# Kernel tuning notes

Measured on AMD Instinct MI355X. Metric: run time of the kernel, lower is better.

## Reference

```python
import jax, jax.numpy as jnp
import numpy as np

B, C, H, W = 8, 256, 64, 64
CI = 128  # inter_channels = in_channels // reduction

def _conv1x1(x, w, b):
    # x: [b, c, h, w], w: [o, c], b: [o]
    return jnp.einsum('bchw,oc->bohw', x, w) + b[None, :, None, None]

def setup_inputs() -> dict:
    key = jax.random.key(0)
    ks = jax.random.split(key, 5)
    s_in = 1.0 / np.sqrt(C)
    s_ci = 1.0 / np.sqrt(CI)
    return {
        'x': jax.random.normal(ks[0], (B, C, H, W), jnp.float32),
        'w_g': jax.random.normal(ks[1], (CI, C), jnp.float32) * s_in,
        'b_g': jnp.zeros((CI,), jnp.float32),
        'w_theta': jax.random.normal(ks[2], (CI, C), jnp.float32) * s_in,
        'b_theta': jnp.zeros((CI,), jnp.float32),
        'w_phi': jax.random.normal(ks[3], (CI, C), jnp.float32) * s_in,
        'b_phi': jnp.zeros((CI,), jnp.float32),
        'w_out': jax.random.normal(ks[4], (C, CI), jnp.float32) * s_ci,
        'b_out': jnp.zeros((C,), jnp.float32),
    }

def reference(x, w_g, b_g, w_theta, b_theta, w_phi, b_phi, w_out, b_out):
    n, c, h, w = x.shape
    N = h * w
    g_x = _conv1x1(x, w_g, b_g).reshape(n, CI, N).transpose(0, 2, 1)        # [b, N, ci]
    theta_x = _conv1x1(x, w_theta, b_theta).reshape(n, CI, N).transpose(0, 2, 1)  # [b, N, ci]
    phi_x = _conv1x1(x, w_phi, b_phi).reshape(n, CI, N)                     # [b, ci, N]
    pw = jnp.einsum('bnc,bcm->bnm', theta_x, phi_x)                         # [b, N, N]
    # Faithful to source: divides by ci**(-0.5) == multiplies by sqrt(ci)
    pw = pw / (jnp.asarray(CI, x.dtype) ** -0.5)
    pw = jax.nn.softmax(pw, axis=-1)
    y = jnp.einsum('bnm,bmc->bnc', pw, g_x)                                 # [b, N, ci]
    y = y.transpose(0, 2, 1).reshape(n, CI, h, w)
    return x + _conv1x1(y, w_out, b_out)
```

## Files before the change

kernel.cpp:

```cpp
#include <hip/hip_runtime.h>
#include <hip/hip_bf16.h>
#include <stdint.h>
#include <stddef.h>


typedef __bf16 bf16;
typedef __attribute__((ext_vector_type(8))) __bf16 bf16x8;
typedef __attribute__((ext_vector_type(4))) __bf16 bf16x4;
typedef __attribute__((ext_vector_type(4))) float  f32x4;
typedef __attribute__((ext_vector_type(4))) int    i32x4;

#define MFMA16(a, b, c) __builtin_amdgcn_mfma_f32_16x16x32_bf16((a), (b), (c), 0, 0, 0)

constexpr int NB  = 8;
constexpr int NC  = 256;
constexpr int NN  = 4096;
constexpr int NCI = 128;
constexpr size_t NEL = (size_t)NB * NN * NCI;
constexpr int PBATCH = NN * NCI;

#define QSCALE (11.313708498984761f * 1.4426950408889634f)


__global__ __launch_bounds__(256) void k_proj3(
    const float* __restrict__ x,
    const float* __restrict__ wt, const float* __restrict__ bt,
    const float* __restrict__ wp, const float* __restrict__ bp,
    const float* __restrict__ wg, const float* __restrict__ bg,
    bf16* __restrict__ qh, bf16* __restrict__ ql,
    bf16* __restrict__ kh, bf16* __restrict__ kl,
    bf16* __restrict__ vv)
{
    const int nt  = blockIdx.x;
    const int b   = blockIdx.y;
    const int tid = threadIdx.x;
    const int wv  = tid >> 6;
    const int ln  = tid & 63;
    const int lg  = ln >> 4;
    const int lq  = ln & 15;

    __shared__ char lds[49152];
    char* Ah = lds;
    char* Al = lds + 8192;
    char* Wh = lds + 16384;
    char* Wl = lds + 32768;

    f32x4 acc[3][8];
#pragma unroll
    for (int pj = 0; pj < 3; ++pj)
#pragma unroll
        for (int j = 0; j < 8; ++j) acc[pj][j] = f32x4{0.f, 0.f, 0.f, 0.f};

    const int n0 = nt * 64;

    for (int c0 = 0; c0 < NC; c0 += 64) {
        __syncthreads();
#pragma unroll
        for (int p = 0; p < 4; ++p) {
            int cc = p * 16 + (tid >> 4);
            int nn = (tid & 15) * 4;
            f32x4 xv = *(const f32x4*)(x + ((size_t)b * NC + (c0 + cc)) * NN + n0 + nn);
#pragma unroll
            for (int e = 0; e < 4; ++e) {
                float f = xv[e];
                bf16 hh = (bf16)f;
                int row = nn + e;
                int off = (row * 128 + cc * 2) ^ ((row & 7) << 4);
                *(bf16*)(Ah + off) = hh;
                *(bf16*)(Al + off) = (bf16)(f - (float)hh);
            }
        }

#pragma unroll
        for (int pj = 0; pj < 3; ++pj) {
            const float* W = (pj == 0) ? wt : (pj == 1) ? wp : wg;
            const bool split = (pj != 2);
            if (pj != 0) __syncthreads();
#pragma unroll
            for (int p = 0; p < 8; ++p) {
                int i  = p * 16 + (tid >> 4);
                int c4 = (tid & 15) * 4;
                f32x4 w4 = *(const f32x4*)(W + (size_t)i * NC + c0 + c4);
                bf16x4 hv, lv;
#pragma unroll
                for (int e = 0; e < 4; ++e) {
                    bf16 hh = (bf16)w4[e];
                    hv[e] = hh;
                    lv[e] = (bf16)(w4[e] - (float)hh);
                }
                int off = (i * 128 + c4 * 2) ^ ((i & 7) << 4);
                *(bf16x4*)(Wh + off) = hv;
                if (split) *(bf16x4*)(Wl + off) = lv;
            }
            __syncthreads();
#pragma unroll
            for (int kk = 0; kk < 2; ++kk) {
                int row  = wv * 16 + lq;
                int koff = kk * 64 + lg * 16;
                int aoff = (row * 128 + koff) ^ ((row & 7) << 4);
                bf16x8 ah = *(const bf16x8*)(Ah + aoff);
                bf16x8 al = *(const bf16x8*)(Al + aoff);
#pragma unroll
                for (int j = 0; j < 8; ++j) {
                    int ir   = j * 16 + lq;
                    int woff = (ir * 128 + koff) ^ ((ir & 7) << 4);
                    bf16x8 bh = *(const bf16x8*)(Wh + woff);
                    acc[pj][j] = MFMA16(ah, bh, acc[pj][j]);
                    if (split) {
                        bf16x8 bl = *(const bf16x8*)(Wl + woff);
                        acc[pj][j] = MFMA16(ah, bl, acc[pj][j]);
                        acc[pj][j] = MFMA16(al, bh, acc[pj][j]);
                    }
                }
            }
        }
    }

#pragma unroll
    for (int j = 0; j < 8; ++j) {
        int i = j * 16 + lq;
        float bvt = bt[i];
        float bvp = bp[i];
#pragma unroll
        for (int r = 0; r < 4; ++r) {
            int q = n0 + wv * 16 + lg * 4 + r;
            size_t off = ((size_t)b * NN + q) * NCI + i;
            float vt2 = (acc[0][j][r] + bvt) * QSCALE;
            bf16 th = (bf16)vt2;
            qh[off] = th; ql[off] = (bf16)(vt2 - (float)th);
            float vp2 = acc[1][j][r] + bvp;
            bf16 phh = (bf16)vp2;
            kh[off] = phh; kl[off] = (bf16)(vp2 - (float)phh);
        }
    }

    __syncthreads();
    char* T = lds;
#pragma unroll
    for (int j = 0; j < 8; ++j) {
        int i = j * 16 + lq;
        float bv2 = bg[i];
#pragma unroll
        for (int r = 0; r < 4; ++r) {
            int nl = wv * 16 + lg * 4 + r;
            int off = (i * 128 + nl * 2) ^ ((i & 7) << 4);
            *(bf16*)(T + off) = (bf16)(acc[2][j][r] + bv2);
        }
    }
    __syncthreads();
#pragma unroll
    for (int p = 0; p < 4; ++p) {
        int i  = p * 32 + (tid >> 3);
        int sl = tid & 7;
        i32x4 tv = *(const i32x4*)(T + ((i * 128 + sl * 16) ^ ((i & 7) << 4)));
        size_t off = (size_t)b * PBATCH
                   + (size_t)((((nt * 8 + (i >> 4)) * 2 + (sl >> 2)) * 64
                               + (sl & 3) * 16 + (i & 15)) * 8);
        *(i32x4*)(vv + off) = tv;
    }
}

__global__ __launch_bounds__(128, 2) void k_attn_sp(
    const bf16* __restrict__ qh, const bf16* __restrict__ ql,
    const bf16* __restrict__ kh, const bf16* __restrict__ kl,
    const bf16* __restrict__ vf,
    bf16* __restrict__ p0, bf16* __restrict__ p1, float* __restrict__ ml)
{
    const int bid = blockIdx.x;
    const int b   = bid & 7;
    const int rs  = bid >> 3;
    const int qt  = rs & 63;
    const int h   = rs >> 6;
    const int tid = threadIdx.x;
    const int wv  = tid >> 6;
    const int ln  = tid & 63;
    const int lg  = ln >> 4;
    const int lq  = ln & 15;
    const int n0  = qt * 64;
    const int mb0 = h * 2048;
    bf16* ph = h ? p1 : p0;

    __shared__ __attribute__((aligned(16))) char lds[36864];
    char* P = lds + 32768 + wv * 2048;

    const int smm = tid >> 4;
    const int ssl = tid & 15;

    bf16x8 qhf[2][4], qlf[2][4];
#pragma unroll
    for (int q2 = 0; q2 < 2; ++q2) {
        int qrow = n0 + wv * 32 + q2 * 16 + lq;
        const bf16* bh = qh + ((size_t)b * NN + qrow) * NCI;
        const bf16* bl = ql + ((size_t)b * NN + qrow) * NCI;
#pragma unroll
        for (int kk = 0; kk < 4; ++kk) {
            qhf[q2][kk] = *(const bf16x8*)(bh + kk * 32 + lg * 8);
            qlf[q2][kk] = *(const bf16x8*)(bl + kk * 32 + lg * 8);
        }
    }

    f32x4 o[2][8];
#pragma unroll
    for (int q2 = 0; q2 < 2; ++q2)
#pragma unroll
        for (int j = 0; j < 8; ++j) o[q2][j] = f32x4{0.f, 0.f, 0.f, 0.f};
    float mrun[2] = {-1e30f, -1e30f};
    float lrun[2] = {0.f, 0.f};

    const bf16* vb = vf + (size_t)b * PBATCH + (size_t)ln * 8;

    {
#pragma unroll
        for (int p = 0; p < 4; ++p) {
            int mm = p * 8 + smm;
            size_t g = ((size_t)b * NN + mb0 + mm) * NCI + ssl * 8;
            i32x4 hv = *(const i32x4*)(kh + g);
            i32x4 lv = *(const i32x4*)(kl + g);
            int off = (mm * 256 + ssl * 16) ^ ((mm & 7) << 4);
            *(i32x4*)(lds + off) = hv;
            *(i32x4*)(lds + 8192 + off) = lv;
        }
    }
    __syncthreads();

    for (int t = 0; t < 64; ++t) {
        const int cur = t & 1;
        char* KHc = lds + cur * 16384;
        char* KLc = KHc + 8192;
        char* KHn = lds + (cur ^ 1) * 16384;
        char* KLn = KHn + 8192;
        const bool pre = (t < 63);

        i32x4 rkh[4], rkl[4];
        if (pre) {
#pragma unroll
            for (int p = 0; p < 4; ++p) {
                size_t g = ((size_t)b * NN + mb0 + (t + 1) * 32 + p * 8 + smm) * NCI + ssl * 8;
                rkh[p] = *(const i32x4*)(kh + g);
                rkl[p] = *(const i32x4*)(kl + g);
            }
        }
        __builtin_amdgcn_sched_barrier(0);

        f32x4 s[2][2];
        __builtin_amdgcn_s_setprio(1);
#pragma unroll
        for (int jm = 0; jm < 2; ++jm) {
            s[jm][0] = f32x4{0.f, 0.f, 0.f, 0.f};
            s[jm][1] = f32x4{0.f, 0.f, 0.f, 0.f};
            const int mrow = jm * 16 + lq;
            const int sw = (mrow & 7) << 4;
#pragma unroll
            for (int kk = 0; kk < 4; ++kk) {
                int aoff = (mrow * 256 + kk * 64 + lg * 16) ^ sw;
                bf16x8 ah = *(const bf16x8*)(KHc + aoff);
                bf16x8 al = *(const bf16x8*)(KLc + aoff);
                s[jm][0] = MFMA16(ah, qhf[0][kk], s[jm][0]);
                s[jm][1] = MFMA16(ah, qhf[1][kk], s[jm][1]);
                s[jm][0] = MFMA16(al, qhf[0][kk], s[jm][0]);
                s[jm][1] = MFMA16(al, qhf[1][kk], s[jm][1]);
                s[jm][0] = MFMA16(ah, qlf[0][kk], s[jm][0]);
                s[jm][1] = MFMA16(ah, qlf[1][kk], s[jm][1]);
            }
        }
        __builtin_amdgcn_s_setprio(0);

        bf16x8 bv[8];
        {
            const bf16* vp = vb + (size_t)(h * 32 + (t >> 1)) * 8192;
#pragma unroll
            for (int j = 0; j < 8; ++j)
                bv[j] = *(const bf16x8*)(vp + (j * 2 + (t & 1)) * 512);
        }
        __builtin_amdgcn_sched_barrier(0);

        if (pre) {
#pragma unroll
            for (int p = 0; p < 4; ++p) {
                int mm = p * 8 + smm;
                int off = (mm * 256 + ssl * 16) ^ ((mm & 7) << 4);
                *(i32x4*)(KHn + off) = rkh[p];
                *(i32x4*)(KLn + off) = rkl[p];
            }
        }

        float tm[2];
        tm[0] = s[0][0][0];
        tm[1] = s[0][1][0];
#pragma unroll
        for (int jm = 0; jm < 2; ++jm)
#pragma unroll
            for (int r = 0; r < 4; ++r) {
                tm[0] = fmaxf(tm[0], s[jm][0][r]);
                tm[1] = fmaxf(tm[1], s[jm][1][r]);
            }
#pragma unroll
        for (int q2 = 0; q2 < 2; ++q2) {
            tm[q2] = fmaxf(tm[q2], __shfl_xor(tm[q2], 16));
            tm[q2] = fmaxf(tm[q2], __shfl_xor(tm[q2], 32));
        }

        bool grow = (tm[0] > mrun[0] + 8.f) || (tm[1] > mrun[1] + 8.f);
        if (__any(grow)) {
            float alpha[2];
#pragma unroll
            for (int q2 = 0; q2 < 2; ++q2) {
                float mnew = fmaxf(mrun[q2], tm[q2]);
                alpha[q2] = exp2f(mrun[q2] - mnew);
                mrun[q2] = mnew;
                lrun[q2] *= alpha[q2];
            }
            float av0[4], av1[4];
#pragma unroll
            for (int r = 0; r < 4; ++r) {
                av0[r] = __shfl(alpha[0], lg * 4 + r);
                av1[r] = __shfl(alpha[1], lg * 4 + r);
            }
#pragma unroll
            for (int j = 0; j < 8; ++j)
#pragma unroll
                for (int r = 0; r < 4; ++r) {
                    o[0][j][r] *= av0[r];
                    o[1][j][r] *= av1[r];
                }
        }

        float psum[2] = {0.f, 0.f};
#pragma unroll
        for (int jm = 0; jm < 2; ++jm)
#pragma unroll
            for (int q2 = 0; q2 < 2; ++q2) {
                bf16x4 pk;
#pragma unroll
                for (int r = 0; r < 4; ++r) {
                    float e2 = exp2f(s[jm][q2][r] - mrun[q2]);
                    psum[q2] += e2;
                    pk[r] = (bf16)e2;
                }
                int row = q2 * 16 + lq;
                int off = (row * 64 + (jm * 16 + lg * 4) * 2) ^ ((row & 7) << 4);
                *(bf16x4*)(P + off) = pk;
            }
#pragma unroll
        for (int q2 = 0; q2 < 2; ++q2) {
            psum[q2] += __shfl_xor(psum[q2], 16);
            psum[q2] += __shfl_xor(psum[q2], 32);
            lrun[q2] += psum[q2];
        }

        bf16x8 pa[2];
#pragma unroll
        for (int q2 = 0; q2 < 2; ++q2) {
            int row = q2 * 16 + lq;
            pa[q2] = *(const bf16x8*)(P + ((row * 64 + lg * 16) ^ ((row & 7) << 4)));
        }
        __builtin_amdgcn_s_setprio(1);
#pragma unroll
        for (int j = 0; j < 8; ++j) {
            o[0][j] = MFMA16(pa[0], bv[j], o[0][j]);
            o[1][j] = MFMA16(pa[1], bv[j], o[1][j]);
        }
        __builtin_amdgcn_s_setprio(0);

        __syncthreads();
    }

    float rl0[4], rl1[4];
#pragma unroll
    for (int r = 0; r < 4; ++r) {
        rl0[r] = 1.f / __shfl(lrun[0], lg * 4 + r);
        rl1[r] = 1.f / __shfl(lrun[1], lg * 4 + r);
    }
#pragma unroll
    for (int j = 0; j < 8; ++j) {
        int d = j * 16 + lq;
#pragma unroll
        for (int r = 0; r < 4; ++r) {
            int q0 = n0 + wv * 32 + lg * 4 + r;
            ph[((size_t)b * NN + q0) * NCI + d]      = (bf16)(o[0][j][r] * rl0[r]);
            ph[((size_t)b * NN + q0 + 16) * NCI + d] = (bf16)(o[1][j][r] * rl1[r]);
        }
    }
    if (lg == 0) {
#pragma unroll
        for (int q2 = 0; q2 < 2; ++q2) {
            int row = n0 + wv * 32 + q2 * 16 + lq;
            size_t base = ((size_t)b * NN + row) * 4 + h * 2;
            ml[base]     = mrun[q2];
            ml[base + 1] = lrun[q2];
        }
    }
}

__global__ __launch_bounds__(256) void k_out(
    const bf16* __restrict__ p0, const bf16* __restrict__ p1,
    const float* __restrict__ ml, const float* __restrict__ x,
    const float* __restrict__ w_out, const float* __restrict__ b_out,
    float* __restrict__ out)
{
    const int nt  = blockIdx.x;
    const int b   = blockIdx.y;
    const int tid = threadIdx.x;
    const int wv  = tid >> 6;
    const int ln  = tid & 63;
    const int lg  = ln >> 4;
    const int lq  = ln & 15;
    const int n0  = nt * 64;

    __shared__ char Y[16384];
#pragma unroll
    for (int p = 0; p < 4; ++p) {
        int nn = p * 16 + (tid >> 4);
        int d0 = (tid & 15) * 8;
        size_t row = (size_t)b * NN + n0 + nn;
        f32x4 q = *(const f32x4*)(ml + row * 4);
        float M  = fmaxf(q[0], q[2]);
        float w0 = exp2f(q[0] - M) * q[1];
        float w1 = exp2f(q[2] - M) * q[3];
        float inv = 1.f / (w0 + w1);
        w0 *= inv; w1 *= inv;
        size_t off = row * NCI + d0;
        bf16x8 a = *(const bf16x8*)(p0 + off);
        bf16x8 c = *(const bf16x8*)(p1 + off);
        bf16x8 rr;
#pragma unroll
        for (int e = 0; e < 8; ++e)
            rr[e] = (bf16)(w0 * (float)a[e] + w1 * (float)c[e]);
        *(bf16x8*)(Y + ((nn * 256 + d0 * 2) ^ ((nn & 7) << 4))) = rr;
    }
    __syncthreads();

    bf16x8 af[4];
    {
        int row = wv * 16 + lq;
#pragma unroll
        for (int kk = 0; kk < 4; ++kk) {
            int koff = kk * 64 + lg * 16;
            af[kk] = *(const bf16x8*)(Y + ((row * 256 + koff) ^ ((row & 7) << 4)));
        }
    }

    f32x4 acc[16];
#pragma unroll
    for (int j = 0; j < 16; ++j) acc[j] = f32x4{0.f, 0.f, 0.f, 0.f};

#pragma unroll
    for (int j = 0; j < 16; ++j) {
        int c = j * 16 + lq;
#pragma unroll
        for (int kk = 0; kk < 4; ++kk) {
            int i0 = kk * 32 + lg * 8;
            f32x4 wa = *(const f32x4*)(w_out + (size_t)c * NCI + i0);
            f32x4 wb = *(const f32x4*)(w_out + (size_t)c * NCI + i0 + 4);
            bf16x8 bw;
#pragma unroll
            for (int e = 0; e < 4; ++e) { bw[e] = (bf16)wa[e]; bw[e + 4] = (bf16)wb[e]; }
            acc[j] = MFMA16(af[kk], bw, acc[j]);
        }
    }

#pragma unroll
    for (int j = 0; j < 16; ++j) {
        int c = j * 16 + lq;
        int nb = n0 + wv * 16 + lg * 4;
        size_t off = ((size_t)b * NC + c) * (size_t)NN + nb;
        f32x4 xv = *(const f32x4*)(x + off);
        float bo = b_out[c];
        f32x4 r;
#pragma unroll
        for (int t = 0; t < 4; ++t) r[t] = acc[j][t] + xv[t] + bo;
        *(f32x4*)(out + off) = r;
    }
}

extern "C" void kernel_launch(void* const* d_in, const int* in_sizes, int n_in,
                              void* d_out, int out_size, void* d_ws, size_t ws_size,
                              hipStream_t stream)
{
    (void)in_sizes; (void)n_in; (void)out_size; (void)ws_size;
    const float* x  = (const float*)d_in[0];
    const float* wg = (const float*)d_in[1];
    const float* bg = (const float*)d_in[2];
    const float* wt = (const float*)d_in[3];
    const float* bt = (const float*)d_in[4];
    const float* wp = (const float*)d_in[5];
    const float* bp = (const float*)d_in[6];
    const float* wo = (const float*)d_in[7];
    const float* bo = (const float*)d_in[8];
    float* out = (float*)d_out;

    char* ws = (char*)d_ws;
    bf16* qh = (bf16*)(ws);
    bf16* ql = (bf16*)(ws + NEL * 2);
    bf16* kh = (bf16*)(ws + NEL * 4);
    bf16* kl = (bf16*)(ws + NEL * 6);
    bf16* vv = (bf16*)(ws + NEL * 8);
    bf16* p0 = (bf16*)(ws + NEL * 10);
    bf16* p1 = (bf16*)(ws + NEL * 12);
    float* ml = (float*)(ws + NEL * 14);

    k_proj3<<<dim3(64, 8), 256, 0, stream>>>(x, wt, bt, wp, bp, wg, bg,
                                             qh, ql, kh, kl, vv);
    k_attn_sp<<<dim3(1024), 128, 0, stream>>>(qh, ql, kh, kl, vv, p0, p1, ml);
    k_out<<<dim3(64, 8), 256, 0, stream>>>(p0, p1, ml, x, wo, bo, out);
}
```

Before: 247.2 us.

## Enlarge attention tiles to 128 queries x 64 keys and pre-convert w_out to bf16

The attention kernel now uses 256-thread blocks covering 128 query rows, and processes 64 keys per iteration instead of 32. This halves the number of loop iterations and the grid size, and each K tile loaded into LDS is reused by twice as many queries. LDS use grows to 80KB, which may limit blocks per CU. Separately, the projection kernel converts w_out to bf16 once into workspace when space allows, so the output kernel reads bf16 weights instead of converting fp32 per block.

```diff
diff --git a/kernel.cpp b/kernel.cpp
--- a/kernel.cpp
+++ b/kernel.cpp
@@ -27,6 +27,7 @@
     const float* __restrict__ wt, const float* __restrict__ bt,
     const float* __restrict__ wp, const float* __restrict__ bp,
     const float* __restrict__ wg, const float* __restrict__ bg,
+    const float* __restrict__ wo, bf16* __restrict__ wob,
     bf16* __restrict__ qh, bf16* __restrict__ ql,
     bf16* __restrict__ kh, bf16* __restrict__ kl,
     bf16* __restrict__ vv)
@@ -39,6 +40,15 @@
     const int lg  = ln >> 4;
     const int lq  = ln & 15;
 
+    if (wob != nullptr && tid < 16) {
+        int idx = (b * 64 + nt) * 64 + tid * 4;
+        f32x4 w4 = *(const f32x4*)(wo + idx);
+        bf16x4 o4;
+#pragma unroll
+        for (int e = 0; e < 4; ++e) o4[e] = (bf16)w4[e];
+        *(bf16x4*)(wob + idx) = o4;
+    }
+
     __shared__ char lds[49152];
     char* Ah = lds;
     char* Al = lds + 8192;
@@ -160,7 +170,7 @@
     }
 }
 
-__global__ __launch_bounds__(128, 2) void k_attn_sp(
+__global__ __launch_bounds__(256, 2) void k_attn_sp(
     const bf16* __restrict__ qh, const bf16* __restrict__ ql,
     const bf16* __restrict__ kh, const bf16* __restrict__ kl,
     const bf16* __restrict__ vf,
@@ -169,19 +179,19 @@
     const int bid = blockIdx.x;
     const int b   = bid & 7;
     const int rs  = bid >> 3;
-    const int qt  = rs & 63;
-    const int h   = rs >> 6;
+    const int qt  = rs & 31;
+    const int h   = rs >> 5;
     const int tid = threadIdx.x;
     const int wv  = tid >> 6;
     const int ln  = tid & 63;
     const int lg  = ln >> 4;
     const int lq  = ln & 15;
-    const int n0  = qt * 64;
+    const int n0  = qt * 128;
     const int mb0 = h * 2048;
     bf16* ph = h ? p1 : p0;
 
-    __shared__ __attribute__((aligned(16))) char lds[36864];
-    char* P = lds + 32768 + wv * 2048;
+    __shared__ __attribute__((aligned(16))) char lds[81920];
+    char* P = lds + 65536 + wv * 4096;
 
     const int smm = tid >> 4;
     const int ssl = tid & 15;
@@ -212,40 +222,40 @@
     {
 #pragma unroll
         for (int p = 0; p < 4; ++p) {
-            int mm = p * 8 + smm;
+            int mm = p * 16 + smm;
             size_t g = ((size_t)b * NN + mb0 + mm) * NCI + ssl * 8;
             i32x4 hv = *(const i32x4*)(kh + g);
             i32x4 lv = *(const i32x4*)(kl + g);
             int off = (mm * 256 + ssl * 16) ^ ((mm & 7) << 4);
             *(i32x4*)(lds + off) = hv;
-            *(i32x4*)(lds + 8192 + off) = lv;
+            *(i32x4*)(lds + 16384 + off) = lv;
         }
     }
     __syncthreads();
 
-    for (int t = 0; t < 64; ++t) {
+    for (int t = 0; t < 32; ++t) {
         const int cur = t & 1;
-        char* KHc = lds + cur * 16384;
-        char* KLc = KHc + 8192;
-        char* KHn = lds + (cur ^ 1) * 16384;
-        char* KLn = KHn + 8192;
-        const bool pre = (t < 63);
+        char* KHc = lds + cur * 32768;
+        char* KLc = KHc + 16384;
+        char* KHn = lds + (cur ^ 1) * 32768;
+        char* KLn = KHn + 16384;
+        const bool pre = (t < 31);
 
         i32x4 rkh[4], rkl[4];
         if (pre) {
 #pragma unroll
             for (int p = 0; p < 4; ++p) {
-                size_t g = ((size_t)b * NN + mb0 + (t + 1) * 32 + p * 8 + smm) * NCI + ssl * 8;
+                size_t g = ((size_t)b * NN + mb0 + (t + 1) * 64 + p * 16 + smm) * NCI + ssl * 8;
                 rkh[p] = *(const i32x4*)(kh + g);
                 rkl[p] = *(const i32x4*)(kl + g);
             }
         }
         __builtin_amdgcn_sched_barrier(0);
 
-        f32x4 s[2][2];
+        f32x4 s[4][2];
         __builtin_amdgcn_s_setprio(1);
 #pragma unroll
-        for (int jm = 0; jm < 2; ++jm) {
+        for (int jm = 0; jm < 4; ++jm) {
             s[jm][0] = f32x4{0.f, 0.f, 0.f, 0.f};
             s[jm][1] = f32x4{0.f, 0.f, 0.f, 0.f};
             const int mrow = jm * 16 + lq;
@@ -265,19 +275,21 @@
         }
         __builtin_amdgcn_s_setprio(0);
 
-        bf16x8 bv[8];
+        bf16x8 bv[8][2];
         {
-            const bf16* vp = vb + (size_t)(h * 32 + (t >> 1)) * 8192;
-#pragma unroll
-            for (int j = 0; j < 8; ++j)
-                bv[j] = *(const bf16x8*)(vp + (j * 2 + (t & 1)) * 512);
+            const bf16* vp = vb + (size_t)(h * 32 + t) * 8192;
+#pragma unroll
+            for (int j = 0; j < 8; ++j) {
+                bv[j][0] = *(const bf16x8*)(vp + (j * 2 + 0) * 512);
+                bv[j][1] = *(const bf16x8*)(vp + (j * 2 + 1) * 512);
+            }
         }
         __builtin_amdgcn_sched_barrier(0);
 
         if (pre) {
 #pragma unroll
             for (int p = 0; p < 4; ++p) {
-                int mm = p * 8 + smm;
+                int mm = p * 16 + smm;
                 int off = (mm * 256 + ssl * 16) ^ ((mm & 7) << 4);
                 *(i32x4*)(KHn + off) = rkh[p];
                 *(i32x4*)(KLn + off) = rkl[p];
@@ -288,7 +300,7 @@
         tm[0] = s[0][0][0];
         tm[1] = s[0][1][0];
 #pragma unroll
-        for (int jm = 0; jm < 2; ++jm)
+        for (int jm = 0; jm < 4; ++jm)
 #pragma unroll
             for (int r = 0; r < 4; ++r) {
                 tm[0] = fmaxf(tm[0], s[jm][0][r]);
@@ -327,7 +339,7 @@
 
         float psum[2] = {0.f, 0.f};
 #pragma unroll
-        for (int jm = 0; jm < 2; ++jm)
+        for (int jm = 0; jm < 4; ++jm)
 #pragma unroll
             for (int q2 = 0; q2 < 2; ++q2) {
                 bf16x4 pk;
@@ -338,7 +350,7 @@
                     pk[r] = (bf16)e2;
                 }
                 int row = q2 * 16 + lq;
-                int off = (row * 64 + (jm * 16 + lg * 4) * 2) ^ ((row & 7) << 4);
+                int off = (row * 128 + (jm * 16 + lg * 4) * 2) ^ ((row & 7) << 4);
                 *(bf16x4*)(P + off) = pk;
             }
 #pragma unroll
@@ -348,17 +360,21 @@
             lrun[q2] += psum[q2];
         }
 
-        bf16x8 pa[2];
-#pragma unroll
-        for (int q2 = 0; q2 < 2; ++q2) {
-            int row = q2 * 16 + lq;
-            pa[q2] = *(const bf16x8*)(P + ((row * 64 + lg * 16) ^ ((row & 7) << 4)));
-        }
+        bf16x8 pa[2][2];
+#pragma unroll
+        for (int q2 = 0; q2 < 2; ++q2)
+#pragma unroll
+            for (int tt = 0; tt < 2; ++tt) {
+                int row = q2 * 16 + lq;
+                pa[q2][tt] = *(const bf16x8*)(P + ((row * 128 + tt * 64 + lg * 16) ^ ((row & 7) << 4)));
+            }
         __builtin_amdgcn_s_setprio(1);
 #pragma unroll
         for (int j = 0; j < 8; ++j) {
-            o[0][j] = MFMA16(pa[0], bv[j], o[0][j]);
-            o[1][j] = MFMA16(pa[1], bv[j], o[1][j]);
+            o[0][j] = MFMA16(pa[0][0], bv[j][0], o[0][j]);
+            o[1][j] = MFMA16(pa[1][0], bv[j][0], o[1][j]);
+            o[0][j] = MFMA16(pa[0][1], bv[j][1], o[0][j]);
+            o[1][j] = MFMA16(pa[1][1], bv[j][1], o[1][j]);
         }
         __builtin_amdgcn_s_setprio(0);
 
@@ -395,8 +411,8 @@
 __global__ __launch_bounds__(256) void k_out(
     const bf16* __restrict__ p0, const bf16* __restrict__ p1,
     const float* __restrict__ ml, const float* __restrict__ x,
-    const float* __restrict__ w_out, const float* __restrict__ b_out,
-    float* __restrict__ out)
+    const float* __restrict__ w_out, const bf16* __restrict__ wob,
+    const float* __restrict__ b_out, float* __restrict__ out)
 {
     const int nt  = blockIdx.x;
     const int b   = blockIdx.y;
@@ -444,18 +460,31 @@
 #pragma unroll
     for (int j = 0; j < 16; ++j) acc[j] = f32x4{0.f, 0.f, 0.f, 0.f};
 
-#pragma unroll
-    for (int j = 0; j < 16; ++j) {
-        int c = j * 16 + lq;
-#pragma unroll
-        for (int kk = 0; kk < 4; ++kk) {
-            int i0 = kk * 32 + lg * 8;
-            f32x4 wa = *(const f32x4*)(w_out + (size_t)c * NCI + i0);
-            f32x4 wb = *(const f32x4*)(w_out + (size_t)c * NCI + i0 + 4);
-            bf16x8 bw;
-#pragma unroll
-            for (int e = 0; e < 4; ++e) { bw[e] = (bf16)wa[e]; bw[e + 4] = (bf16)wb[e]; }
-            acc[j] = MFMA16(af[kk], bw, acc[j]);
+    if (wob != nullptr) {
+#pragma unroll
+        for (int j = 0; j < 16; ++j) {
+            int c = j * 16 + lq;
+#pragma unroll
+            for (int kk = 0; kk < 4; ++kk) {
+                int i0 = kk * 32 + lg * 8;
+                bf16x8 bw = *(const bf16x8*)(wob + (size_t)c * NCI + i0);
+                acc[j] = MFMA16(af[kk], bw, acc[j]);
+            }
+        }
+    } else {
+#pragma unroll
+        for (int j = 0; j < 16; ++j) {
+            int c = j * 16 + lq;
+#pragma unroll
+            for (int kk = 0; kk < 4; ++kk) {
+                int i0 = kk * 32 + lg * 8;
+                f32x4 wa = *(const f32x4*)(w_out + (size_t)c * NCI + i0);
+                f32x4 wb = *(const f32x4*)(w_out + (size_t)c * NCI + i0 + 4);
+                bf16x8 bw;
+#pragma unroll
+                for (int e = 0; e < 4; ++e) { bw[e] = (bf16)wa[e]; bw[e + 4] = (bf16)wb[e]; }
+                acc[j] = MFMA16(af[kk], bw, acc[j]);
+            }
         }
     }
 
@@ -477,7 +506,7 @@
                               void* d_out, int out_size, void* d_ws, size_t ws_size,
                               hipStream_t stream)
 {
-    (void)in_sizes; (void)n_in; (void)out_size; (void)ws_size;
+    (void)in_sizes; (void)n_in; (void)out_size;
     const float* x  = (const float*)d_in[0];
     const float* wg = (const float*)d_in[1];
     const float* bg = (const float*)d_in[2];
@@ -498,9 +527,13 @@
     bf16* p0 = (bf16*)(ws + NEL * 10);
     bf16* p1 = (bf16*)(ws + NEL * 12);
     float* ml = (float*)(ws + NEL * 14);
+    const size_t ml_bytes = (size_t)NB * NN * 4 * sizeof(float);
+    bf16* wob = nullptr;
+    if (ws_size >= NEL * 14 + ml_bytes + (size_t)NC * NCI * sizeof(bf16))
+        wob = (bf16*)(ws + NEL * 14 + ml_bytes);
 
     k_proj3<<<dim3(64, 8), 256, 0, stream>>>(x, wt, bt, wp, bp, wg, bg,
-                                             qh, ql, kh, kl, vv);
-    k_attn_sp<<<dim3(1024), 128, 0, stream>>>(qh, ql, kh, kl, vv, p0, p1, ml);
-    k_out<<<dim3(64, 8), 256, 0, stream>>>(p0, p1, ml, x, wo, bo, out);
+                                             wo, wob, qh, ql, kh, kl, vv);
+    k_attn_sp<<<dim3(512), 256, 0, stream>>>(qh, ql, kh, kl, vv, p0, p1, ml);
+    k_out<<<dim3(64, 8), 256, 0, stream>>>(p0, p1, ml, x, wo, wob, bo, out);
 }
```

New measurement: 370.9 us. 1.5x slower.
